# Kernel optimization log

Hardware: AMD Instinct MI355X
Metric: run time of the kernel (lower is better)

Reference implementation:

```python
import jax, jax.numpy as jnp
import numpy as np

C = 256   # in_channels
H = 48
W = 48
B = 2     # batch after chunking into 3 frames; input batch = 3*B
F = 3     # frames (torch.chunk(x, 3))
G = 4     # GroupNorm groups
EPS = 1e-6


def setup_inputs() -> dict:
    key = jax.random.key(0)
    ks = jax.random.split(key, 10)
    s = C ** -0.5  # keep q/k magnitudes sane so softmax is not saturated
    return {
        "x":    jax.random.normal(ks[0], (F * B, C, H, W), jnp.float32),
        "gn_w": jnp.ones((C,), jnp.float32),
        "gn_b": jnp.zeros((C,), jnp.float32),
        "wq":   jax.random.normal(ks[1], (C, C), jnp.float32) * s,
        "bq":   jax.random.normal(ks[2], (C,), jnp.float32) * 0.02,
        "wk":   jax.random.normal(ks[3], (C, C), jnp.float32) * s,
        "bk":   jax.random.normal(ks[4], (C,), jnp.float32) * 0.02,
        "wv":   jax.random.normal(ks[5], (C, C), jnp.float32) * s,
        "bv":   jax.random.normal(ks[6], (C,), jnp.float32) * 0.02,
        "wp":   jax.random.normal(ks[7], (C, C), jnp.float32) * s,
        "bp":   jax.random.normal(ks[8], (C,), jnp.float32) * 0.02,
    }


def reference(x, gn_w, gn_b, wq, bq, wk, bk, wv, bv, wp, bp):
    B3, c, h, w = x.shape
    b = B3 // F
    # torch.chunk(x, 3) + stack(dim=2) -> (b, c, f, h, w); chunk index is frame
    hx = jnp.moveaxis(x.reshape(F, b, c, h, w), 0, 2)  # (b, c, f, h, w)

    # GroupNorm(num_groups=4, eps=1e-6, affine)
    hg = hx.reshape(b, G, c // G, F, h, w)
    mu = hg.mean(axis=(2, 3, 4, 5), keepdims=True)
    var = hg.var(axis=(2, 3, 4, 5), keepdims=True)
    hn = ((hg - mu) * jax.lax.rsqrt(var + EPS)).reshape(b, c, F, h, w)
    hn = hn * gn_w[None, :, None, None, None] + gn_b[None, :, None, None, None]

    # 1x1x1 Conv3d == channel matmul over flattened tokens n = (f h w)
    n = F * h * w
    hf = hn.reshape(b, c, n)                                  # (b, c, n)
    q = jnp.einsum('oc,bcn->bon', wq, hf) + bq[None, :, None]
    k = jnp.einsum('oc,bcn->bon', wk, hf) + bk[None, :, None]
    v = jnp.einsum('oc,bcn->bon', wv, hf) + bv[None, :, None]

    # scores[b,n,m] = sum_c q[b,c,n] * k[b,c,m], scaled by c^-0.5, softmax over m
    scores = jnp.einsum('bcn,bcm->bnm', q, k) * (c ** -0.5)
    attn = jax.nn.softmax(scores, axis=-1)                    # (b, n, n)

    # out[b,c,n] = sum_m v[b,c,m] * attn[b,n,m]
    o = jnp.einsum('bcm,bnm->bcn', v, attn)
    o = jnp.einsum('oc,bcn->bon', wp, o) + bp[None, :, None]  # proj_out

    o = o.reshape(b, c, F, h, w)
    # permute(0,2,1,3,4) then merge (b f) -> batch (b-major, f-minor)
    o = jnp.moveaxis(o, 2, 1).reshape(B3, c, h, w)
    return x + o
```

## Files before the change

kernel.cpp:

```cpp
#include <hip/hip_runtime.h>
#include <stdint.h>

#define CDIM 256
#define HW 2304
#define FR 3
#define NBATCH 2
#define NTOK 6912
#define EPSV 1e-6f
#define LOG2E 1.44269504088896f
#define QSCALE (0.0625f * 1.44269504088896f)

typedef __attribute__((ext_vector_type(8))) short short8;
typedef __attribute__((ext_vector_type(4))) float f32x4;
typedef unsigned short u16;

__device__ inline u16 f2bf(float f) {
  union { float f; uint32_t u; } v; v.f = f;
  uint32_t r = v.u + 0x7FFFu + ((v.u >> 16) & 1u);
  return (u16)(r >> 16);
}
__device__ inline float bf2f(u16 h) {
  union { uint32_t u; float f; } v; v.u = ((uint32_t)h) << 16; return v.f;
}
__device__ inline void gload16(const void* g, void* l) {
  __builtin_amdgcn_global_load_lds(
      (const __attribute__((address_space(1))) void*)g,
      (__attribute__((address_space(3))) void*)l, 16, 0, 0);
}

__global__ void cvt_w_k(const float* wq, const float* wk, const float* wv,
                        const float* wp, u16* wb) {
  int idx = blockIdx.x * 256 + threadIdx.x;
  wb[0 * 65536 + idx] = f2bf(wq[idx] * QSCALE);
  wb[1 * 65536 + idx] = f2bf(wk[idx]);
  wb[2 * 65536 + idx] = f2bf(wv[idx]);
  wb[3 * 65536 + idx] = f2bf(wp[idx]);
}

__global__ void gn_part_k(const float* x, float* part) {
  int bg = blockIdx.x >> 5, sl = blockIdx.x & 31;
  int b = bg >> 2, g = bg & 3;
  int tid = threadIdx.x;
  float s1 = 0.f, s2 = 0.f;
  for (int i = tid; i < 2 * NTOK; i += 256) {
    int cl = sl * 2 + (i / NTOK); int rem = i % NTOK;
    int f = rem / HW; int hw = rem - f * HW;
    float v = x[((size_t)(f * NBATCH + b) * CDIM + g * 64 + cl) * HW + hw];
    s1 += v; s2 += v * v;
  }
  #pragma unroll
  for (int m = 32; m >= 1; m >>= 1) {
    s1 += __shfl_xor(s1, m, 64);
    s2 += __shfl_xor(s2, m, 64);
  }
  __shared__ float r1[4], r2[4];
  int wid = tid >> 6;
  if ((tid & 63) == 0) { r1[wid] = s1; r2[wid] = s2; }
  __syncthreads();
  if (tid == 0) {
    part[blockIdx.x * 2 + 0] = r1[0] + r1[1] + r1[2] + r1[3];
    part[blockIdx.x * 2 + 1] = r2[0] + r2[1] + r2[2] + r2[3];
  }
}

__global__ void gn_fin_k(const float* part, float* stats) {
  int tid = threadIdx.x;
  if (tid < 8) {
    float s1 = 0.f, s2 = 0.f;
    for (int s = 0; s < 32; ++s) {
      s1 += part[(tid * 32 + s) * 2 + 0];
      s2 += part[(tid * 32 + s) * 2 + 1];
    }
    float inv = 1.f / (64.f * NTOK);
    float mu = s1 * inv;
    float var = s2 * inv - mu * mu;
    stats[tid * 2 + 0] = mu;
    stats[tid * 2 + 1] = rsqrtf(var + EPSV);
  }
}

__global__ void gn_apply_k(const float* x, const float* gn_w, const float* gn_b,
                           const float* stats, u16* hn) {
  int nt = blockIdx.x, ct = blockIdx.y, b = blockIdx.z;
  int tid = threadIdx.x;
  __shared__ float tile[64][65];
  int n0 = nt * 64; int f = n0 / HW; int hw0 = n0 - f * HW;
  float mu = stats[(b * 4 + ct) * 2 + 0];
  float rs = stats[(b * 4 + ct) * 2 + 1];
  #pragma unroll
  for (int i = 0; i < 16; ++i) {
    int lin = i * 256 + tid;
    int cr = lin >> 6, nc = lin & 63;
    int c = ct * 64 + cr;
    float v = x[((size_t)(f * NBATCH + b) * CDIM + c) * HW + hw0 + nc];
    tile[cr][nc] = (v - mu) * rs * gn_w[c] + gn_b[c];
  }
  __syncthreads();
  #pragma unroll
  for (int i = 0; i < 16; ++i) {
    int lin = i * 256 + tid;
    int nr = lin >> 6, cc = lin & 63;
    hn[((size_t)b * NTOK + n0 + nr) * CDIM + ct * 64 + cc] = f2bf(tile[cc][nr]);
  }
}

__global__ __launch_bounds__(256) void qkv_k(const u16* hn, const u16* wb,
    const float* bq, const float* bk, const float* bv,
    u16* qb, u16* kb, u16* vb) {
  int nt = blockIdx.x;
  int op = blockIdx.y >> 1, b = blockIdx.y & 1;
  int tid = threadIdx.x, lane = tid & 63, wid = tid >> 6;
  int lr = lane & 15, lg = lane >> 4;
  __shared__ __align__(16) char hn_lds[32768];
  {
    const char* src = (const char*)(hn + ((size_t)b * NTOK + nt * 64) * CDIM);
    #pragma unroll
    for (int i = 0; i < 8; ++i) {
      int off = i * 4096 + wid * 1024 + lane * 16;
      int row = off >> 9;
      gload16(src + (off ^ ((row & 7) << 4)), hn_lds + i * 4096 + wid * 1024);
    }
  }
  __syncthreads();
  f32x4 acc[16];
  #pragma unroll
  for (int i = 0; i < 16; ++i) acc[i] = (f32x4){0.f, 0.f, 0.f, 0.f};
  const u16* wsrc = wb + op * 65536;
  __builtin_amdgcn_s_setprio(1);
  #pragma unroll
  for (int cc = 0; cc < 4; ++cc) {
    short8 afr[2];
    #pragma unroll
    for (int kc = 0; kc < 2; ++kc) {
      int row = wid * 16 + lr;
      int byte = row * 512 + (cc * 64 + kc * 32 + lg * 8) * 2;
      afr[kc] = *(const short8*)(hn_lds + (byte ^ ((row & 7) << 4)));
    }
    #pragma unroll
    for (int cot = 0; cot < 16; ++cot) {
      #pragma unroll
      for (int kc = 0; kc < 2; ++kc) {
        short8 bfr = *(const short8*)(wsrc + (size_t)(cot * 16 + lr) * CDIM +
                                      cc * 64 + kc * 32 + lg * 8);
        acc[cot] = __builtin_amdgcn_mfma_f32_16x16x32_bf16(afr[kc], bfr, acc[cot], 0, 0, 0);
      }
    }
  }
  __builtin_amdgcn_s_setprio(0);
  const float* bias = (op == 0) ? bq : (op == 1) ? bk : bv;
  float bscale = (op == 0) ? QSCALE : 1.0f;
  int nbase = nt * 64 + wid * 16 + lg * 4;
  #pragma unroll
  for (int cot = 0; cot < 16; ++cot) {
    int co = cot * 16 + lr;
    float bv_ = bias[co] * bscale;
    #pragma unroll
    for (int j = 0; j < 4; ++j) {
      float val = acc[cot][j] + bv_;
      int n = nbase + j;
      if (op == 2) {
        int tile = n >> 6, m = n & 63;
        int slot = ((m >> 3) + co) & 7;
        vb[(size_t)b * NTOK * CDIM + (size_t)tile * 16384 + co * 64 +
           slot * 8 + (m & 7)] = f2bf(val);
      } else if (op == 1) {
        int tile = n >> 6, row = n & 63;
        int slot = ((co >> 3) + 2 * row) & 31;
        kb[(size_t)b * NTOK * CDIM + (size_t)tile * 16384 + row * 256 +
           slot * 8 + (co & 7)] = f2bf(val);
      } else {
        qb[((size_t)b * NTOK + n) * CDIM + co] = f2bf(val);
      }
    }
  }
}

template <int TPB, bool SPLIT>
__global__ __launch_bounds__(512, 2) void flash_k(const u16* qb, const u16* kb,
                                                  const u16* vb, u16* opart,
                                                  float* ml, u16* ob) {
  int qt = blockIdx.x, b = blockIdx.y, sp = blockIdx.z;
  int tid = threadIdx.x, lane = tid & 63, wid = tid >> 6;
  int lr = lane & 15, lg = lane >> 4;
  __shared__ __align__(16) char k_lds[2][32768];
  __shared__ __align__(16) char v_lds[2][32768];
  __shared__ __align__(16) char p_lds[8][2048];

  short8 aq[8];
  int nq = qt * 128 + wid * 16 + lr;
  const u16* qsrc = qb + ((size_t)b * NTOK + nq) * CDIM;
  #pragma unroll
  for (int kc = 0; kc < 8; ++kc) aq[kc] = *(const short8*)(qsrc + kc * 32 + lg * 8);

  float mrun = -1e30f, lrun = 0.f;
  f32x4 acc[16];
  #pragma unroll
  for (int i = 0; i < 16; ++i) acc[i] = (f32x4){0.f, 0.f, 0.f, 0.f};

  const char* kbb = (const char*)(kb + (size_t)b * NTOK * CDIM);
  const char* vbb = (const char*)(vb + (size_t)b * NTOK * CDIM);
  char* pw = p_lds[wid];

  {
    const char* ks = kbb + (size_t)(sp * TPB) * 32768;
    const char* vs = vbb + (size_t)(sp * TPB) * 32768;
    #pragma unroll
    for (int i = 0; i < 4; ++i) {
      gload16(ks + wid * 4096 + i * 1024 + lane * 16,
              k_lds[0] + wid * 4096 + i * 1024);
      gload16(vs + wid * 4096 + i * 1024 + lane * 16,
              v_lds[0] + wid * 4096 + i * 1024);
    }
  }
  __syncthreads();

  for (int t = 0; t < TPB; ++t) {
    int cur = t & 1;
    int kt = sp * TPB + t;
    if (t + 1 < TPB) {
      const char* ks = kbb + (size_t)(kt + 1) * 32768;
      const char* vs = vbb + (size_t)(kt + 1) * 32768;
      #pragma unroll
      for (int i = 0; i < 4; ++i) {
        gload16(ks + wid * 4096 + i * 1024 + lane * 16,
                k_lds[cur ^ 1] + wid * 4096 + i * 1024);
        gload16(vs + wid * 4096 + i * 1024 + lane * 16,
                v_lds[cur ^ 1] + wid * 4096 + i * 1024);
      }
    }
    f32x4 s[4];
    __builtin_amdgcn_s_setprio(1);
    #pragma unroll
    for (int mt = 0; mt < 4; ++mt) {
      f32x4 a = (f32x4){0.f, 0.f, 0.f, 0.f};
      #pragma unroll
      for (int kc = 0; kc < 8; ++kc) {
        int row = mt * 16 + lr;
        int slot = (kc * 4 + lg + 2 * row) & 31;
        short8 kf = *(const short8*)(k_lds[cur] + row * 512 + slot * 16);
        a = __builtin_amdgcn_mfma_f32_16x16x32_bf16(kf, aq[kc], a, 0, 0, 0);
      }
      s[mt] = a;
    }
    __builtin_amdgcn_s_setprio(0);
    float m0 = fmaxf(fmaxf(s[0][0], s[0][1]), fmaxf(s[0][2], s[0][3]));
    float m1 = fmaxf(fmaxf(s[1][0], s[1][1]), fmaxf(s[1][2], s[1][3]));
    float m2 = fmaxf(fmaxf(s[2][0], s[2][1]), fmaxf(s[2][2], s[2][3]));
    float m3 = fmaxf(fmaxf(s[3][0], s[3][1]), fmaxf(s[3][2], s[3][3]));
    float pmax = fmaxf(fmaxf(m0, m1), fmaxf(m2, m3));
    pmax = fmaxf(pmax, __shfl_xor(pmax, 16, 64));
    pmax = fmaxf(pmax, __shfl_xor(pmax, 32, 64));
    float mn = mrun;
    if (__any(pmax > mrun + 6.0f)) {
      mn = fmaxf(mrun, pmax);
      float r = exp2f(mrun - mn);
      mrun = mn;
      lrun *= r;
      #pragma unroll
      for (int i = 0; i < 16; ++i) {
        acc[i][0] *= r; acc[i][1] *= r; acc[i][2] *= r; acc[i][3] *= r;
      }
    }
    float ls = 0.f;
    #pragma unroll
    for (int mt = 0; mt < 4; ++mt) {
      #pragma unroll
      for (int j = 0; j < 4; ++j) {
        float p = exp2f(s[mt][j] - mn);
        s[mt][j] = p;
        ls += p;
      }
    }
    ls += __shfl_xor(ls, 16, 64);
    ls += __shfl_xor(ls, 32, 64);
    lrun += ls;
    #pragma unroll
    for (int mt = 0; mt < 4; ++mt) {
      #pragma unroll
      for (int tp = 0; tp < 2; ++tp) {
        uint32_t pk = (uint32_t)f2bf(s[mt][2 * tp]) |
                      ((uint32_t)f2bf(s[mt][2 * tp + 1]) << 16);
        int byte = lr * 128 + mt * 32 + lg * 8 + tp * 4;
        *(uint32_t*)(pw + (byte ^ ((lr & 7) << 4))) = pk;
      }
    }
    __builtin_amdgcn_s_setprio(1);
    #pragma unroll
    for (int mc = 0; mc < 2; ++mc) {
      int pb = lr * 128 + mc * 64 + lg * 16;
      short8 bfr = *(const short8*)(pw + (pb ^ ((lr & 7) << 4)));
      #pragma unroll
      for (int ct = 0; ct < 16; ++ct) {
        int row = ct * 16 + lr;
        int slot = (mc * 4 + lg + row) & 7;
        short8 av = *(const short8*)(v_lds[cur] + row * 128 + slot * 16);
        acc[ct] = __builtin_amdgcn_mfma_f32_16x16x32_bf16(av, bfr, acc[ct], 0, 0, 0);
      }
    }
    __builtin_amdgcn_s_setprio(0);
    __syncthreads();
  }

  int n = qt * 128 + wid * 16 + lr;
  if (!SPLIT) {
    float linv = 1.0f / lrun;
    #pragma unroll
    for (int ct = 0; ct < 16; ++ct) {
      #pragma unroll
      for (int j = 0; j < 4; ++j) {
        int c = ct * 16 + lg * 4 + j;
        ob[((size_t)b * NTOK + n) * CDIM + c] = f2bf(acc[ct][j] * linv);
      }
    }
  } else {
    size_t pbase = (size_t)(sp * 2 + b) * CDIM * NTOK;
    #pragma unroll
    for (int ct = 0; ct < 16; ++ct) {
      #pragma unroll
      for (int j = 0; j < 4; ++j) {
        int c = ct * 16 + lg * 4 + j;
        opart[pbase + (size_t)c * NTOK + n] = f2bf(acc[ct][j]);
      }
    }
    if (lg == 0) {
      ml[((size_t)(sp * 2 + b) * 2 + 0) * NTOK + n] = mrun;
      ml[((size_t)(sp * 2 + b) * 2 + 1) * NTOK + n] = lrun;
    }
  }
}

__global__ __launch_bounds__(256) void comb_k(const u16* opart, const float* ml,
                                              u16* ob) {
  int nt = blockIdx.x, b = blockIdx.y;
  int tid = threadIdx.x;
  int n = nt * 64 + (tid & 63);
  int cchunk = tid >> 6;
  float m0 = ml[((size_t)(0 * 2 + b) * 2 + 0) * NTOK + n];
  float l0 = ml[((size_t)(0 * 2 + b) * 2 + 1) * NTOK + n];
  float m1 = ml[((size_t)(1 * 2 + b) * 2 + 0) * NTOK + n];
  float l1 = ml[((size_t)(1 * 2 + b) * 2 + 1) * NTOK + n];
  float M = fmaxf(m0, m1);
  float w0 = exp2f(m0 - M), w1 = exp2f(m1 - M);
  float inv = 1.f / (w0 * l0 + w1 * l1);
  float a0 = w0 * inv, a1 = w1 * inv;
  const u16* p0 = opart + (size_t)(0 * 2 + b) * CDIM * NTOK;
  const u16* p1 = opart + (size_t)(1 * 2 + b) * CDIM * NTOK;
  u16 buf[64];
  #pragma unroll
  for (int i = 0; i < 64; ++i) {
    int c = cchunk * 64 + i;
    float v = a0 * bf2f(p0[(size_t)c * NTOK + n]) +
              a1 * bf2f(p1[(size_t)c * NTOK + n]);
    buf[i] = f2bf(v);
  }
  #pragma unroll
  for (int i = 0; i < 8; ++i)
    *(short8*)(ob + ((size_t)b * NTOK + n) * CDIM + cchunk * 64 + i * 8) =
        *(const short8*)(buf + i * 8);
}

__global__ __launch_bounds__(256) void proj_k(const u16* ob, const u16* wb,
    const float* bp, const float* x, float* out) {
  int nt = blockIdx.x, b = blockIdx.y, z = blockIdx.z;
  int tid = threadIdx.x, lane = tid & 63, wid = tid >> 6;
  int lr = lane & 15, lg = lane >> 4;
  __shared__ __align__(16) char o_lds[32768];
  const u16* wpb = wb + 3 * 65536;
  {
    const char* src = (const char*)(ob + ((size_t)b * NTOK + nt * 64) * CDIM);
    #pragma unroll
    for (int i = 0; i < 8; ++i) {
      int off = i * 4096 + wid * 1024 + lane * 16;
      int row = off >> 9;
      gload16(src + (off ^ ((row & 7) << 4)), o_lds + i * 4096 + wid * 1024);
    }
  }
  __syncthreads();
  #pragma unroll
  for (int ct2 = 0; ct2 < 2; ++ct2) {
    int cot = z * 8 + wid * 2 + ct2;
    short8 aw[8];
    #pragma unroll
    for (int kc = 0; kc < 8; ++kc)
      aw[kc] = *(const short8*)(wpb + (size_t)(cot * 16 + lr) * CDIM + kc * 32 + lg * 8);
    #pragma unroll
    for (int ntile = 0; ntile < 4; ++ntile) {
      f32x4 a = (f32x4){0.f, 0.f, 0.f, 0.f};
      #pragma unroll
      for (int kc = 0; kc < 8; ++kc) {
        int row = ntile * 16 + lr;
        int byte = row * 512 + (kc * 32 + lg * 8) * 2;
        short8 bfr = *(const short8*)(o_lds + (byte ^ ((row & 7) << 4)));
        a = __builtin_amdgcn_mfma_f32_16x16x32_bf16(aw[kc], bfr, a, 0, 0, 0);
      }
      int n = nt * 64 + ntile * 16 + lr;
      int f = n / HW; int hw = n - f * HW;
      #pragma unroll
      for (int j = 0; j < 4; ++j) {
        int co = cot * 16 + lg * 4 + j;
        float val = a[j] + bp[co];
        size_t oi = ((size_t)(b * FR + f) * CDIM + co) * HW + hw;
        out[oi] = x[oi] + val;
      }
    }
  }
}

extern "C" void kernel_launch(void* const* d_in, const int* in_sizes, int n_in,
                              void* d_out, int out_size, void* d_ws, size_t ws_size,
                              hipStream_t stream) {
  const float* x    = (const float*)d_in[0];
  const float* gn_w = (const float*)d_in[1];
  const float* gn_b = (const float*)d_in[2];
  const float* wq   = (const float*)d_in[3];
  const float* bq   = (const float*)d_in[4];
  const float* wk   = (const float*)d_in[5];
  const float* bk   = (const float*)d_in[6];
  const float* wv   = (const float*)d_in[7];
  const float* bv   = (const float*)d_in[8];
  const float* wp   = (const float*)d_in[9];
  const float* bp   = (const float*)d_in[10];
  float* out = (float*)d_out;
  char* ws = (char*)d_ws;

  float* stats = (float*)(ws + 0);
  float* part  = (float*)(ws + 256);
  u16* wb = (u16*)(ws + 4096);
  u16* hn = (u16*)(ws + 528384);
  u16* qb = (u16*)(ws + 7606272);
  u16* kb = (u16*)(ws + 14684160);
  u16* vb = (u16*)(ws + 21762048);
  u16* ob = (u16*)(ws + 28839936);
  u16* opart = (u16*)(ws + 35917824);
  float* ml  = (float*)(ws + 50073600);
  const size_t NEED_SPLIT = 50294784;

  cvt_w_k<<<256, 256, 0, stream>>>(wq, wk, wv, wp, wb);
  gn_part_k<<<256, 256, 0, stream>>>(x, part);
  gn_fin_k<<<1, 64, 0, stream>>>(part, stats);
  gn_apply_k<<<dim3(108, 4, 2), 256, 0, stream>>>(x, gn_w, gn_b, stats, hn);
  qkv_k<<<dim3(108, 6), 256, 0, stream>>>(hn, wb, bq, bk, bv, qb, kb, vb);
  if (ws_size >= NEED_SPLIT) {
    flash_k<54, true><<<dim3(54, 2, 2), 512, 0, stream>>>(qb, kb, vb, opart, ml, ob);
    comb_k<<<dim3(108, 2), 256, 0, stream>>>(opart, ml, ob);
  } else {
    flash_k<108, false><<<dim3(54, 2, 1), 512, 0, stream>>>(qb, kb, vb, opart, ml, ob);
  }
  proj_k<<<dim3(108, 2, 2), 256, 0, stream>>>(ob, wb, bp, x, out);
}
```

Measured before the change: 267.8 us.

## Use 12-wave flash blocks with 3-way KV split and vectorized stores

Flash attention blocks grow from 8 to 12 waves (192 queries per block), and the key/value range is split three ways instead of two, giving 216 blocks. The partial-output layout becomes token-major, so the combine kernel reads 16-byte vectors across three splits. The QKV epilogue swaps MFMA operand order so each lane stores 4 consecutive bf16 values as one vector. The weight-conversion and GroupNorm partial-sum kernels are merged into one launch. These changes target wave-level parallelism, scattered 2-byte stores and launch overhead, at the cost of more registers and LDS per block and more combine traffic.

```diff
diff --git a/kernel.cpp b/kernel.cpp
--- a/kernel.cpp
+++ b/kernel.cpp
@@ -7,10 +7,10 @@
 #define NBATCH 2
 #define NTOK 6912
 #define EPSV 1e-6f
-#define LOG2E 1.44269504088896f
 #define QSCALE (0.0625f * 1.44269504088896f)
 
 typedef __attribute__((ext_vector_type(8))) short short8;
+typedef __attribute__((ext_vector_type(4))) short short4v;
 typedef __attribute__((ext_vector_type(4))) float f32x4;
 typedef unsigned short u16;
 
@@ -28,16 +28,17 @@
       (__attribute__((address_space(3))) void*)l, 16, 0, 0);
 }
 
-__global__ void cvt_w_k(const float* wq, const float* wk, const float* wv,
-                        const float* wp, u16* wb) {
-  int idx = blockIdx.x * 256 + threadIdx.x;
-  wb[0 * 65536 + idx] = f2bf(wq[idx] * QSCALE);
-  wb[1 * 65536 + idx] = f2bf(wk[idx]);
-  wb[2 * 65536 + idx] = f2bf(wv[idx]);
-  wb[3 * 65536 + idx] = f2bf(wp[idx]);
-}
-
-__global__ void gn_part_k(const float* x, float* part) {
+__global__ void pre_k(const float* x, float* part, const float* wq,
+                      const float* wk, const float* wv, const float* wp,
+                      u16* wb) {
+  if (blockIdx.x >= 256) {
+    int idx = (blockIdx.x - 256) * 256 + threadIdx.x;
+    wb[0 * 65536 + idx] = f2bf(wq[idx] * QSCALE);
+    wb[1 * 65536 + idx] = f2bf(wk[idx]);
+    wb[2 * 65536 + idx] = f2bf(wv[idx]);
+    wb[3 * 65536 + idx] = f2bf(wp[idx]);
+    return;
+  }
   int bg = blockIdx.x >> 5, sl = blockIdx.x & 31;
   int b = bg >> 2, g = bg & 3;
   int tid = threadIdx.x;
@@ -142,41 +143,52 @@
       for (int kc = 0; kc < 2; ++kc) {
         short8 bfr = *(const short8*)(wsrc + (size_t)(cot * 16 + lr) * CDIM +
                                       cc * 64 + kc * 32 + lg * 8);
-        acc[cot] = __builtin_amdgcn_mfma_f32_16x16x32_bf16(afr[kc], bfr, acc[cot], 0, 0, 0);
+        if (op == 2)
+          acc[cot] = __builtin_amdgcn_mfma_f32_16x16x32_bf16(afr[kc], bfr, acc[cot], 0, 0, 0);
+        else
+          acc[cot] = __builtin_amdgcn_mfma_f32_16x16x32_bf16(bfr, afr[kc], acc[cot], 0, 0, 0);
       }
     }
   }
   __builtin_amdgcn_s_setprio(0);
-  const float* bias = (op == 0) ? bq : (op == 1) ? bk : bv;
-  float bscale = (op == 0) ? QSCALE : 1.0f;
-  int nbase = nt * 64 + wid * 16 + lg * 4;
-  #pragma unroll
-  for (int cot = 0; cot < 16; ++cot) {
-    int co = cot * 16 + lr;
-    float bv_ = bias[co] * bscale;
-    #pragma unroll
-    for (int j = 0; j < 4; ++j) {
-      float val = acc[cot][j] + bv_;
-      int n = nbase + j;
-      if (op == 2) {
-        int tile = n >> 6, m = n & 63;
-        int slot = ((m >> 3) + co) & 7;
-        vb[(size_t)b * NTOK * CDIM + (size_t)tile * 16384 + co * 64 +
-           slot * 8 + (m & 7)] = f2bf(val);
-      } else if (op == 1) {
-        int tile = n >> 6, row = n & 63;
+  if (op == 2) {
+    int m0 = wid * 16 + lg * 4;
+    char* vtile = (char*)vb + (size_t)b * NTOK * CDIM * 2 + (size_t)nt * 32768;
+    #pragma unroll
+    for (int cot = 0; cot < 16; ++cot) {
+      int co = cot * 16 + lr;
+      float bb = bv[co];
+      short4v r;
+      #pragma unroll
+      for (int j = 0; j < 4; ++j) r[j] = (short)f2bf(acc[cot][j] + bb);
+      int slot = ((m0 >> 3) + co) & 7;
+      *(short4v*)(vtile + co * 128 + slot * 16 + (m0 & 7) * 2) = r;
+    }
+  } else {
+    int row = wid * 16 + lr;
+    int n = nt * 64 + row;
+    const float* bias = (op == 0) ? bq : bk;
+    float bscale = (op == 0) ? QSCALE : 1.0f;
+    char* ktile = (char*)kb + (size_t)b * NTOK * CDIM * 2 + (size_t)nt * 32768;
+    #pragma unroll
+    for (int cot = 0; cot < 16; ++cot) {
+      int co = cot * 16 + lg * 4;
+      f32x4 b4 = *(const f32x4*)(bias + co);
+      short4v r;
+      #pragma unroll
+      for (int j = 0; j < 4; ++j) r[j] = (short)f2bf(acc[cot][j] + b4[j] * bscale);
+      if (op == 0) {
+        *(short4v*)(qb + ((size_t)b * NTOK + n) * CDIM + co) = r;
+      } else {
         int slot = ((co >> 3) + 2 * row) & 31;
-        kb[(size_t)b * NTOK * CDIM + (size_t)tile * 16384 + row * 256 +
-           slot * 8 + (co & 7)] = f2bf(val);
-      } else {
-        qb[((size_t)b * NTOK + n) * CDIM + co] = f2bf(val);
-      }
-    }
-  }
-}
-
-template <int TPB, bool SPLIT>
-__global__ __launch_bounds__(512, 2) void flash_k(const u16* qb, const u16* kb,
+        *(short4v*)(ktile + row * 512 + slot * 16 + (co & 7) * 2) = r;
+      }
+    }
+  }
+}
+
+template <bool SPLIT>
+__global__ __launch_bounds__(768, 3) void flash_k(const u16* qb, const u16* kb,
                                                   const u16* vb, u16* opart,
                                                   float* ml, u16* ob) {
   int qt = blockIdx.x, b = blockIdx.y, sp = blockIdx.z;
@@ -184,10 +196,13 @@
   int lr = lane & 15, lg = lane >> 4;
   __shared__ __align__(16) char k_lds[2][32768];
   __shared__ __align__(16) char v_lds[2][32768];
-  __shared__ __align__(16) char p_lds[8][2048];
+  __shared__ __align__(16) char p_lds[12][2048];
+
+  int t0 = SPLIT ? 36 * sp : 0;
+  int t1 = SPLIT ? 36 * sp + 36 : 108;
 
   short8 aq[8];
-  int nq = qt * 128 + wid * 16 + lr;
+  int nq = qt * 192 + wid * 16 + lr;
   const u16* qsrc = qb + ((size_t)b * NTOK + nq) * CDIM;
   #pragma unroll
   for (int kc = 0; kc < 8; ++kc) aq[kc] = *(const short8*)(qsrc + kc * 32 + lg * 8);
@@ -202,30 +217,23 @@
   char* pw = p_lds[wid];
 
   {
-    const char* ks = kbb + (size_t)(sp * TPB) * 32768;
-    const char* vs = vbb + (size_t)(sp * TPB) * 32768;
-    #pragma unroll
-    for (int i = 0; i < 4; ++i) {
-      gload16(ks + wid * 4096 + i * 1024 + lane * 16,
-              k_lds[0] + wid * 4096 + i * 1024);
-      gload16(vs + wid * 4096 + i * 1024 + lane * 16,
-              v_lds[0] + wid * 4096 + i * 1024);
+    const char* ks = kbb + (size_t)t0 * 32768;
+    const char* vs = vbb + (size_t)t0 * 32768;
+    for (int ch = wid; ch < 64; ch += 12) {
+      if (ch < 32) gload16(ks + ch * 1024 + lane * 16, k_lds[0] + ch * 1024);
+      else gload16(vs + (ch - 32) * 1024 + lane * 16, v_lds[0] + (ch - 32) * 1024);
     }
   }
   __syncthreads();
 
-  for (int t = 0; t < TPB; ++t) {
-    int cur = t & 1;
-    int kt = sp * TPB + t;
-    if (t + 1 < TPB) {
-      const char* ks = kbb + (size_t)(kt + 1) * 32768;
-      const char* vs = vbb + (size_t)(kt + 1) * 32768;
-      #pragma unroll
-      for (int i = 0; i < 4; ++i) {
-        gload16(ks + wid * 4096 + i * 1024 + lane * 16,
-                k_lds[cur ^ 1] + wid * 4096 + i * 1024);
-        gload16(vs + wid * 4096 + i * 1024 + lane * 16,
-                v_lds[cur ^ 1] + wid * 4096 + i * 1024);
+  for (int t = t0; t < t1; ++t) {
+    int cur = (t - t0) & 1;
+    if (t + 1 < t1) {
+      const char* ks = kbb + (size_t)(t + 1) * 32768;
+      const char* vs = vbb + (size_t)(t + 1) * 32768;
+      for (int ch = wid; ch < 64; ch += 12) {
+        if (ch < 32) gload16(ks + ch * 1024 + lane * 16, k_lds[cur ^ 1] + ch * 1024);
+        else gload16(vs + (ch - 32) * 1024 + lane * 16, v_lds[cur ^ 1] + (ch - 32) * 1024);
       }
     }
     f32x4 s[4];
@@ -250,12 +258,10 @@
     float pmax = fmaxf(fmaxf(m0, m1), fmaxf(m2, m3));
     pmax = fmaxf(pmax, __shfl_xor(pmax, 16, 64));
     pmax = fmaxf(pmax, __shfl_xor(pmax, 32, 64));
-    float mn = mrun;
     if (__any(pmax > mrun + 6.0f)) {
-      mn = fmaxf(mrun, pmax);
+      float mn = fmaxf(mrun, pmax);
       float r = exp2f(mrun - mn);
-      mrun = mn;
-      lrun *= r;
+      mrun = mn; lrun *= r;
       #pragma unroll
       for (int i = 0; i < 16; ++i) {
         acc[i][0] *= r; acc[i][1] *= r; acc[i][2] *= r; acc[i][3] *= r;
@@ -266,7 +272,7 @@
     for (int mt = 0; mt < 4; ++mt) {
       #pragma unroll
       for (int j = 0; j < 4; ++j) {
-        float p = exp2f(s[mt][j] - mn);
+        float p = exp2f(s[mt][j] - mrun);
         s[mt][j] = p;
         ls += p;
       }
@@ -301,30 +307,29 @@
     __syncthreads();
   }
 
-  int n = qt * 128 + wid * 16 + lr;
   if (!SPLIT) {
     float linv = 1.0f / lrun;
+    u16* d0 = ob + ((size_t)b * NTOK + nq) * CDIM;
     #pragma unroll
     for (int ct = 0; ct < 16; ++ct) {
-      #pragma unroll
-      for (int j = 0; j < 4; ++j) {
-        int c = ct * 16 + lg * 4 + j;
-        ob[((size_t)b * NTOK + n) * CDIM + c] = f2bf(acc[ct][j] * linv);
-      }
+      short4v r;
+      #pragma unroll
+      for (int j = 0; j < 4; ++j) r[j] = (short)f2bf(acc[ct][j] * linv);
+      *(short4v*)(d0 + ct * 16 + lg * 4) = r;
     }
   } else {
-    size_t pbase = (size_t)(sp * 2 + b) * CDIM * NTOK;
+    u16* d0 = opart + ((size_t)(sp * 2 + b) * NTOK + nq) * CDIM;
     #pragma unroll
     for (int ct = 0; ct < 16; ++ct) {
-      #pragma unroll
-      for (int j = 0; j < 4; ++j) {
-        int c = ct * 16 + lg * 4 + j;
-        opart[pbase + (size_t)c * NTOK + n] = f2bf(acc[ct][j]);
-      }
+      short4v r;
+      #pragma unroll
+      for (int j = 0; j < 4; ++j) r[j] = (short)f2bf(acc[ct][j]);
+      *(short4v*)(d0 + ct * 16 + lg * 4) = r;
     }
     if (lg == 0) {
-      ml[((size_t)(sp * 2 + b) * 2 + 0) * NTOK + n] = mrun;
-      ml[((size_t)(sp * 2 + b) * 2 + 1) * NTOK + n] = lrun;
+      size_t mb = (size_t)(sp * 2 + b) * 2;
+      ml[(mb + 0) * NTOK + nq] = mrun;
+      ml[(mb + 1) * NTOK + nq] = lrun;
     }
   }
 }
@@ -333,30 +338,33 @@
                                               u16* ob) {
   int nt = blockIdx.x, b = blockIdx.y;
   int tid = threadIdx.x;
-  int n = nt * 64 + (tid & 63);
-  int cchunk = tid >> 6;
-  float m0 = ml[((size_t)(0 * 2 + b) * 2 + 0) * NTOK + n];
-  float l0 = ml[((size_t)(0 * 2 + b) * 2 + 1) * NTOK + n];
-  float m1 = ml[((size_t)(1 * 2 + b) * 2 + 0) * NTOK + n];
-  float l1 = ml[((size_t)(1 * 2 + b) * 2 + 1) * NTOK + n];
-  float M = fmaxf(m0, m1);
-  float w0 = exp2f(m0 - M), w1 = exp2f(m1 - M);
-  float inv = 1.f / (w0 * l0 + w1 * l1);
-  float a0 = w0 * inv, a1 = w1 * inv;
-  const u16* p0 = opart + (size_t)(0 * 2 + b) * CDIM * NTOK;
-  const u16* p1 = opart + (size_t)(1 * 2 + b) * CDIM * NTOK;
-  u16 buf[64];
-  #pragma unroll
-  for (int i = 0; i < 64; ++i) {
-    int c = cchunk * 64 + i;
-    float v = a0 * bf2f(p0[(size_t)c * NTOK + n]) +
-              a1 * bf2f(p1[(size_t)c * NTOK + n]);
-    buf[i] = f2bf(v);
-  }
-  #pragma unroll
-  for (int i = 0; i < 8; ++i)
-    *(short8*)(ob + ((size_t)b * NTOK + n) * CDIM + cchunk * 64 + i * 8) =
-        *(const short8*)(buf + i * 8);
+  #pragma unroll
+  for (int g = 0; g < 8; ++g) {
+    int n = nt * 64 + g * 8 + (tid >> 5);
+    int c0 = (tid & 31) * 8;
+    float m[3], l[3];
+    #pragma unroll
+    for (int s = 0; s < 3; ++s) {
+      m[s] = ml[((size_t)(s * 2 + b) * 2 + 0) * NTOK + n];
+      l[s] = ml[((size_t)(s * 2 + b) * 2 + 1) * NTOK + n];
+    }
+    float M = fmaxf(fmaxf(m[0], m[1]), m[2]);
+    float w[3]; float den = 0.f;
+    #pragma unroll
+    for (int s = 0; s < 3; ++s) { w[s] = exp2f(m[s] - M); den += w[s] * l[s]; }
+    float inv = 1.f / den;
+    float o[8] = {0.f, 0.f, 0.f, 0.f, 0.f, 0.f, 0.f, 0.f};
+    #pragma unroll
+    for (int s = 0; s < 3; ++s) {
+      short8 v = *(const short8*)(opart + ((size_t)(s * 2 + b) * NTOK + n) * CDIM + c0);
+      #pragma unroll
+      for (int j = 0; j < 8; ++j) o[j] += w[s] * bf2f((u16)v[j]);
+    }
+    short8 r8;
+    #pragma unroll
+    for (int j = 0; j < 8; ++j) r8[j] = (short)f2bf(o[j] * inv);
+    *(short8*)(ob + ((size_t)b * NTOK + n) * CDIM + c0) = r8;
+  }
 }
 
 __global__ __launch_bounds__(256) void proj_k(const u16* ob, const u16* wb,
@@ -432,19 +440,18 @@
   u16* vb = (u16*)(ws + 21762048);
   u16* ob = (u16*)(ws + 28839936);
   u16* opart = (u16*)(ws + 35917824);
-  float* ml  = (float*)(ws + 50073600);
-  const size_t NEED_SPLIT = 50294784;
-
-  cvt_w_k<<<256, 256, 0, stream>>>(wq, wk, wv, wp, wb);
-  gn_part_k<<<256, 256, 0, stream>>>(x, part);
+  float* ml  = (float*)(ws + 57151488);
+  const size_t NEED_SPLIT = 57483264;
+
+  pre_k<<<512, 256, 0, stream>>>(x, part, wq, wk, wv, wp, wb);
   gn_fin_k<<<1, 64, 0, stream>>>(part, stats);
   gn_apply_k<<<dim3(108, 4, 2), 256, 0, stream>>>(x, gn_w, gn_b, stats, hn);
   qkv_k<<<dim3(108, 6), 256, 0, stream>>>(hn, wb, bq, bk, bv, qb, kb, vb);
   if (ws_size >= NEED_SPLIT) {
-    flash_k<54, true><<<dim3(54, 2, 2), 512, 0, stream>>>(qb, kb, vb, opart, ml, ob);
+    flash_k<true><<<dim3(36, 2, 3), 768, 0, stream>>>(qb, kb, vb, opart, ml, ob);
     comb_k<<<dim3(108, 2), 256, 0, stream>>>(opart, ml, ob);
   } else {
-    flash_k<108, false><<<dim3(54, 2, 1), 512, 0, stream>>>(qb, kb, vb, opart, ml, ob);
+    flash_k<false><<<dim3(36, 2, 1), 768, 0, stream>>>(qb, kb, vb, opart, ml, ob);
   }
   proj_k<<<dim3(108, 2, 2), 256, 0, stream>>>(ob, wb, bp, x, out);
 }
```

New measurement: 229.3 us. 1.17x faster.
